# Optimization experiments

Measured on AMD Instinct MI355X. Metric: run time of the kernel, lower is better.

## Reference

```python
import jax, jax.numpy as jnp
import numpy as np

H = 512
B = 64
S = 2048
NUM_LAYERS = 1


def setup_inputs() -> dict:
    key = jax.random.key(0)
    ks = jax.random.split(key, 8)
    scale = 1.0 / np.sqrt(H)
    return {
        "hidden": jax.random.normal(ks[0], (NUM_LAYERS, B, H), dtype=jnp.float32),
        "encoder_outputs": jax.random.normal(ks[1], (B, S, H), dtype=jnp.float32),
        "U_w": jax.random.uniform(ks[2], (H, H), jnp.float32, -scale, scale),
        "U_b": jax.random.uniform(ks[3], (H,), jnp.float32, -scale, scale),
        "W_w": jax.random.uniform(ks[4], (H, H), jnp.float32, -scale, scale),
        "W_b": jax.random.uniform(ks[5], (H,), jnp.float32, -scale, scale),
        "V_w": jax.random.uniform(ks[6], (1, H), jnp.float32, -scale, scale),
        "V_b": jax.random.uniform(ks[7], (1,), jnp.float32, -scale, scale),
    }


def reference(hidden, encoder_outputs, U_w, U_b, W_w, W_b, V_w, V_b):
    # hidden: [L, B, H] -> take last layer, like hidden[-1]
    h = hidden[-1]  # [B, H]
    # Uatt(h): [B, H] -> broadcast over src_len
    u = h @ U_w.T + U_b            # [B, H]
    w = jnp.einsum('bsh,kh->bsk', encoder_outputs, W_w) + W_b  # [B, S, H]
    combined = jnp.tanh(u[:, None, :] + w)                     # [B, S, H]
    energy = jnp.einsum('bsh,h->bs', combined, V_w[0]) + V_b[0]  # [B, S]
    attn = jax.nn.softmax(energy, axis=1)                       # [B, S]
    context = jnp.einsum('bs,bsh->bh', attn, encoder_outputs)   # [B, H]
    return (context, attn)
```

## Files before the change

kernel.cpp:

```cpp
#include <hip/hip_runtime.h>
#include <hip/hip_bf16.h>

#define H 512
#define B 64
#define S 2048

typedef __bf16 bf16x8 __attribute__((ext_vector_type(8)));
typedef float f32x4 __attribute__((ext_vector_type(4)));
typedef unsigned int u32x4 __attribute__((ext_vector_type(4)));

__device__ __forceinline__ unsigned cvt2(float x, float y) {
    union { __hip_bfloat162 h; unsigned u; } cv;
    cv.h = __float22bfloat162_rn(make_float2(x, y));
    return cv.u;
}

__device__ __forceinline__ float fast_tanh(float x) {
    float e = __expf(2.0f * x);
    float r = __builtin_amdgcn_rcpf(e + 1.0f);
    return 1.0f - 2.0f * r;
}

__device__ __forceinline__ void gload_lds16(const void* g, void* l) {
    __builtin_amdgcn_global_load_lds(
        (const __attribute__((address_space(1))) unsigned int*)g,
        (__attribute__((address_space(3))) unsigned int*)l, 16, 0, 0);
}

__global__ __launch_bounds__(256) void w16_kernel(const float* __restrict__ Ww,
                                                  unsigned short* __restrict__ w16) {
    const int i = (blockIdx.x * 256 + threadIdx.x) * 8;
    float4 a = *(const float4*)(Ww + i);
    float4 b = *(const float4*)(Ww + i + 4);
    uint4 p;
    p.x = cvt2(a.x, a.y); p.y = cvt2(a.z, a.w);
    p.z = cvt2(b.x, b.y); p.w = cvt2(b.z, b.w);
    *(uint4*)(w16 + i) = p;
}

__global__ __launch_bounds__(256) void u_kernel(
        const float* __restrict__ hid, const float* __restrict__ Uw,
        const float* __restrict__ Ub, const float* __restrict__ Wb,
        float* __restrict__ u) {
    const int b = blockIdx.y;
    const int k = blockIdx.x * 4 + (threadIdx.x >> 6);
    const int lane = threadIdx.x & 63;
    const float4* wrow = (const float4*)(Uw + (size_t)k * H);
    const float4* hrow = (const float4*)(hid + (size_t)b * H);
    float4 w0 = wrow[lane * 2], w1 = wrow[lane * 2 + 1];
    float4 h0 = hrow[lane * 2], h1 = hrow[lane * 2 + 1];
    float acc = w0.x * h0.x + w0.y * h0.y + w0.z * h0.z + w0.w * h0.w
              + w1.x * h1.x + w1.y * h1.y + w1.z * h1.z + w1.w * h1.w;
    #pragma unroll
    for (int off = 1; off < 64; off <<= 1) acc += __shfl_xor(acc, off, 64);
    if (lane == 0) u[b * H + k] = acc + Ub[k] + Wb[k];
}

#define CN  32
#define NCH 16
#define CHB (CN * H * 2)

__global__ __launch_bounds__(256, 2) void energy_kernel(
        const float* __restrict__ enc, const unsigned short* __restrict__ w16,
        const float* __restrict__ Vw, const float* __restrict__ u,
        float* __restrict__ energy) {
    const int s0  = blockIdx.x * 128;
    const int b   = blockIdx.y;
    const int tid = threadIdx.x;
    const int wave = tid >> 6, lane = tid & 63;
    const int quad = lane >> 4, c = lane & 15;

    __shared__ unsigned char Bs[2][CHB];
    __shared__ float uS[H], vS[H];

    #pragma unroll
    for (int i = 0; i < 8; ++i) {
        const int row = i * 4 + wave;
        const int d   = (row << 10) + lane * 16;
        gload_lds16((const unsigned char*)w16 + (d ^ ((row & 7) << 4)),
                    &Bs[0][row << 10]);
    }

    for (int i = tid; i < H; i += 256) { uS[i] = u[b * H + i]; vS[i] = Vw[i]; }

    u32x4 apack[2][16];
    #pragma unroll
    for (int g = 0; g < 2; ++g) {
        const float* pa = enc + ((size_t)(b * S + s0 + wave * 32 + g * 16 + c)) * H + quad * 8;
        #pragma unroll
        for (int half = 0; half < 2; ++half) {
            float4 x0[8], x1[8];
            #pragma unroll
            for (int q = 0; q < 8; ++q) {
                const int t = half * 8 + q;
                x0[q] = *(const float4*)(pa + t * 32);
                x1[q] = *(const float4*)(pa + t * 32 + 4);
            }
            #pragma unroll
            for (int q = 0; q < 8; ++q) {
                u32x4 p;
                p[0] = cvt2(x0[q].x, x0[q].y); p[1] = cvt2(x0[q].z, x0[q].w);
                p[2] = cvt2(x1[q].x, x1[q].y); p[3] = cvt2(x1[q].z, x1[q].w);
                apack[g][half * 8 + q] = p;
            }
        }
    }
    #pragma unroll
    for (int g = 0; g < 2; ++g)
        #pragma unroll
        for (int t = 0; t < 16; ++t)
            asm volatile("" : "+v"(apack[g][t]));

    float esum[2][4] = {};
    const int mask = (c & 7) << 4;

    #pragma unroll 2
    for (int cc = 0; cc < NCH; ++cc) {
        const int buf = cc & 1;
        if (cc) __syncthreads();
        if (cc < NCH - 1) {
            const unsigned char* src = (const unsigned char*)w16 + (cc + 1) * CHB;
            #pragma unroll
            for (int i = 0; i < 8; ++i) {
                const int row = i * 4 + wave;
                const int d   = (row << 10) + lane * 16;
                gload_lds16(src + (d ^ ((row & 7) << 4)), &Bs[buf ^ 1][row << 10]);
            }
            asm volatile("s_waitcnt vmcnt(8)" ::: "memory");
        } else {
            asm volatile("s_waitcnt vmcnt(0)" ::: "memory");
        }
        __syncthreads();

        const unsigned char* bb = Bs[buf];
        f32x4 acc[2][2] = {};
        #pragma unroll
        for (int t = 0; t < 16; ++t) {
            const int base = t * 64 + quad * 16;
            bf16x8 b0 = *(const bf16x8*)(bb + ((( c       << 10) + base) ^ mask));
            bf16x8 b1 = *(const bf16x8*)(bb + ((((16 + c) << 10) + base) ^ mask));
            acc[0][0] = __builtin_amdgcn_mfma_f32_16x16x32_bf16(*(const bf16x8*)&apack[0][t], b0, acc[0][0], 0, 0, 0);
            acc[1][0] = __builtin_amdgcn_mfma_f32_16x16x32_bf16(*(const bf16x8*)&apack[1][t], b0, acc[1][0], 0, 0, 0);
            acc[0][1] = __builtin_amdgcn_mfma_f32_16x16x32_bf16(*(const bf16x8*)&apack[0][t], b1, acc[0][1], 0, 0, 0);
            acc[1][1] = __builtin_amdgcn_mfma_f32_16x16x32_bf16(*(const bf16x8*)&apack[1][t], b1, acc[1][1], 0, 0, 0);
        }
        #pragma unroll
        for (int ct = 0; ct < 2; ++ct) {
            const int col = cc * CN + ct * 16 + c;
            const float vv = vS[col], uu = uS[col];
            #pragma unroll
            for (int g = 0; g < 2; ++g)
                #pragma unroll
                for (int r = 0; r < 4; ++r)
                    esum[g][r] += vv * fast_tanh(uu + acc[g][ct][r]);
        }
    }

    #pragma unroll
    for (int g = 0; g < 2; ++g)
        #pragma unroll
        for (int r = 0; r < 4; ++r) {
            float e = esum[g][r];
            e += __shfl_xor(e, 1, 64);
            e += __shfl_xor(e, 2, 64);
            e += __shfl_xor(e, 4, 64);
            e += __shfl_xor(e, 8, 64);
            if (c == 0)
                energy[b * S + s0 + wave * 32 + g * 16 + quad * 4 + r] = e;
        }
}

__global__ void softmax_kernel(const float* __restrict__ energy, float* __restrict__ attn) {
    int b = blockIdx.x;
    int t = threadIdx.x;
    const float* e = energy + b * S;
    float v[8];
    float m = -1e30f;
    #pragma unroll
    for (int i = 0; i < 8; ++i) { v[i] = e[t + i * 256]; m = fmaxf(m, v[i]); }
    #pragma unroll
    for (int off = 1; off < 64; off <<= 1) m = fmaxf(m, __shfl_xor(m, off, 64));
    __shared__ float redm[4], reds[4];
    if ((t & 63) == 0) redm[t >> 6] = m;
    __syncthreads();
    m = fmaxf(fmaxf(redm[0], redm[1]), fmaxf(redm[2], redm[3]));
    float s = 0.f;
    #pragma unroll
    for (int i = 0; i < 8; ++i) { v[i] = __expf(v[i] - m); s += v[i]; }
    #pragma unroll
    for (int off = 1; off < 64; off <<= 1) s += __shfl_xor(s, off, 64);
    if ((t & 63) == 0) reds[t >> 6] = s;
    __syncthreads();
    float inv = 1.0f / (reds[0] + reds[1] + reds[2] + reds[3]);
    #pragma unroll
    for (int i = 0; i < 8; ++i) attn[b * S + t + i * 256] = v[i] * inv;
}

#define CCH 128
__global__ __launch_bounds__(256) void context_kernel(
        const float* __restrict__ enc, const float* __restrict__ attn,
        float* __restrict__ ctx) {
    const int b  = blockIdx.x >> 4;
    const int ch = blockIdx.x & 15;
    const int t  = threadIdx.x;
    const int grp = t >> 7;
    const int ln  = t & 127;
    __shared__ float aS[CCH];
    __shared__ float red[H];
    if (t < CCH) aS[t] = attn[b * S + ch * CCH + t];
    __syncthreads();
    const float* ebase = enc + ((size_t)(b * S + ch * CCH) + grp * 64) * H + ln * 4;
    float4 acc = make_float4(0.f, 0.f, 0.f, 0.f);
    #pragma unroll 8
    for (int s = 0; s < 64; ++s) {
        const float a = aS[grp * 64 + s];
        const float4 e = *(const float4*)(ebase + (size_t)s * H);
        acc.x += a * e.x; acc.y += a * e.y; acc.z += a * e.z; acc.w += a * e.w;
    }
    if (grp == 0) *(float4*)&red[ln * 4] = acc;
    __syncthreads();
    if (grp == 1) {
        const float4 r = *(const float4*)&red[ln * 4];
        atomicAdd(&ctx[b * H + ln * 4 + 0], acc.x + r.x);
        atomicAdd(&ctx[b * H + ln * 4 + 1], acc.y + r.y);
        atomicAdd(&ctx[b * H + ln * 4 + 2], acc.z + r.z);
        atomicAdd(&ctx[b * H + ln * 4 + 3], acc.w + r.w);
    }
}

extern "C" void kernel_launch(void* const* d_in, const int* in_sizes, int n_in,
                              void* d_out, int out_size, void* d_ws, size_t ws_size,
                              hipStream_t stream) {
    (void)in_sizes; (void)n_in; (void)out_size; (void)ws_size;
    const float* hid = (const float*)d_in[0];
    const float* enc = (const float*)d_in[1];
    const float* Uw  = (const float*)d_in[2];
    const float* Ub  = (const float*)d_in[3];
    const float* Ww  = (const float*)d_in[4];
    const float* Wb  = (const float*)d_in[5];
    const float* Vw  = (const float*)d_in[6];

    float* out_ctx  = (float*)d_out;
    float* out_attn = out_ctx + B * H;
    float* energy   = (float*)d_ws;
    float* u        = energy + B * S;
    unsigned short* w16 = (unsigned short*)(u + B * H);

    hipMemsetAsync(d_out, 0, (size_t)B * H * sizeof(float), stream);

    w16_kernel<<<dim3(H * H / (256 * 8)), 256, 0, stream>>>(Ww, w16);
    u_kernel<<<dim3(H / 4, B), 256, 0, stream>>>(hid, Uw, Ub, Wb, u);
    energy_kernel<<<dim3(S / 128, B), 256, 0, stream>>>(enc, w16, Vw, u, energy);
    softmax_kernel<<<B, 256, 0, stream>>>(energy, out_attn);
    context_kernel<<<B * 16, 256, 0, stream>>>(enc, out_attn, out_ctx);
}
```

Baseline: 479.8 us.

## Split energy block across 8 waves with 16 rows each to raise occupancy

The energy kernel now runs 512 threads per block. Each wave owns 16 sequence rows instead of 32, which halves the A-fragment registers and accumulators per wave, and the launch bound asks for 4 blocks per CU. The W chunk loads are spread over 8 waves (4 loads each) with a matching vmcnt, and s_setprio is raised around the MFMA loop. The aim is more resident waves to hide LDS and global latency. In exchange, each B fragment read from LDS now feeds only 2 MFMAs instead of 4, so LDS read traffic per FLOP doubles.

Result: slower. 490.6 us (+2.3%).

```diff
diff --git a/kernel.cpp b/kernel.cpp
--- a/kernel.cpp
+++ b/kernel.cpp
@@ -60,7 +60,7 @@
 #define NCH 16
 #define CHB (CN * H * 2)
 
-__global__ __launch_bounds__(256, 2) void energy_kernel(
+__global__ __launch_bounds__(512, 4) void energy_kernel(
         const float* __restrict__ enc, const unsigned short* __restrict__ w16,
         const float* __restrict__ Vw, const float* __restrict__ u,
         float* __restrict__ energy) {
@@ -74,19 +74,19 @@
     __shared__ float uS[H], vS[H];
 
     #pragma unroll
-    for (int i = 0; i < 8; ++i) {
-        const int row = i * 4 + wave;
+    for (int i = 0; i < 4; ++i) {
+        const int row = i * 8 + wave;
         const int d   = (row << 10) + lane * 16;
         gload_lds16((const unsigned char*)w16 + (d ^ ((row & 7) << 4)),
                     &Bs[0][row << 10]);
     }
 
-    for (int i = tid; i < H; i += 256) { uS[i] = u[b * H + i]; vS[i] = Vw[i]; }
-
-    u32x4 apack[2][16];
-    #pragma unroll
-    for (int g = 0; g < 2; ++g) {
-        const float* pa = enc + ((size_t)(b * S + s0 + wave * 32 + g * 16 + c)) * H + quad * 8;
+    uS[tid] = u[b * H + tid];
+    vS[tid] = Vw[tid];
+
+    u32x4 apack[16];
+    {
+        const float* pa = enc + ((size_t)(b * S + s0 + wave * 16 + c)) * H + quad * 8;
         #pragma unroll
         for (int half = 0; half < 2; ++half) {
             float4 x0[8], x1[8];
@@ -101,17 +101,13 @@
                 u32x4 p;
                 p[0] = cvt2(x0[q].x, x0[q].y); p[1] = cvt2(x0[q].z, x0[q].w);
                 p[2] = cvt2(x1[q].x, x1[q].y); p[3] = cvt2(x1[q].z, x1[q].w);
-                apack[g][half * 8 + q] = p;
+                apack[half * 8 + q] = p;
+                asm volatile("" : "+v"(apack[half * 8 + q]));
             }
         }
     }
-    #pragma unroll
-    for (int g = 0; g < 2; ++g)
-        #pragma unroll
-        for (int t = 0; t < 16; ++t)
-            asm volatile("" : "+v"(apack[g][t]));
-
-    float esum[2][4] = {};
+
+    float esum[4] = {};
     const int mask = (c & 7) << 4;
 
     #pragma unroll 2
@@ -121,53 +117,49 @@
         if (cc < NCH - 1) {
             const unsigned char* src = (const unsigned char*)w16 + (cc + 1) * CHB;
             #pragma unroll
-            for (int i = 0; i < 8; ++i) {
-                const int row = i * 4 + wave;
+            for (int i = 0; i < 4; ++i) {
+                const int row = i * 8 + wave;
                 const int d   = (row << 10) + lane * 16;
                 gload_lds16(src + (d ^ ((row & 7) << 4)), &Bs[buf ^ 1][row << 10]);
             }
-            asm volatile("s_waitcnt vmcnt(8)" ::: "memory");
+            asm volatile("s_waitcnt vmcnt(4)" ::: "memory");
         } else {
             asm volatile("s_waitcnt vmcnt(0)" ::: "memory");
         }
         __syncthreads();
 
         const unsigned char* bb = Bs[buf];
-        f32x4 acc[2][2] = {};
+        f32x4 acc[2] = {};
+        __builtin_amdgcn_s_setprio(1);
         #pragma unroll
         for (int t = 0; t < 16; ++t) {
             const int base = t * 64 + quad * 16;
             bf16x8 b0 = *(const bf16x8*)(bb + ((( c       << 10) + base) ^ mask));
             bf16x8 b1 = *(const bf16x8*)(bb + ((((16 + c) << 10) + base) ^ mask));
-            acc[0][0] = __builtin_amdgcn_mfma_f32_16x16x32_bf16(*(const bf16x8*)&apack[0][t], b0, acc[0][0], 0, 0, 0);
-            acc[1][0] = __builtin_amdgcn_mfma_f32_16x16x32_bf16(*(const bf16x8*)&apack[1][t], b0, acc[1][0], 0, 0, 0);
-            acc[0][1] = __builtin_amdgcn_mfma_f32_16x16x32_bf16(*(const bf16x8*)&apack[0][t], b1, acc[0][1], 0, 0, 0);
-            acc[1][1] = __builtin_amdgcn_mfma_f32_16x16x32_bf16(*(const bf16x8*)&apack[1][t], b1, acc[1][1], 0, 0, 0);
-        }
+            acc[0] = __builtin_amdgcn_mfma_f32_16x16x32_bf16(*(const bf16x8*)&apack[t], b0, acc[0], 0, 0, 0);
+            acc[1] = __builtin_amdgcn_mfma_f32_16x16x32_bf16(*(const bf16x8*)&apack[t], b1, acc[1], 0, 0, 0);
+        }
+        __builtin_amdgcn_s_setprio(0);
         #pragma unroll
         for (int ct = 0; ct < 2; ++ct) {
             const int col = cc * CN + ct * 16 + c;
             const float vv = vS[col], uu = uS[col];
             #pragma unroll
-            for (int g = 0; g < 2; ++g)
-                #pragma unroll
-                for (int r = 0; r < 4; ++r)
-                    esum[g][r] += vv * fast_tanh(uu + acc[g][ct][r]);
-        }
-    }
-
-    #pragma unroll
-    for (int g = 0; g < 2; ++g)
-        #pragma unroll
-        for (int r = 0; r < 4; ++r) {
-            float e = esum[g][r];
-            e += __shfl_xor(e, 1, 64);
-            e += __shfl_xor(e, 2, 64);
-            e += __shfl_xor(e, 4, 64);
-            e += __shfl_xor(e, 8, 64);
-            if (c == 0)
-                energy[b * S + s0 + wave * 32 + g * 16 + quad * 4 + r] = e;
-        }
+            for (int r = 0; r < 4; ++r)
+                esum[r] += vv * fast_tanh(uu + acc[ct][r]);
+        }
+    }
+
+    #pragma unroll
+    for (int r = 0; r < 4; ++r) {
+        float e = esum[r];
+        e += __shfl_xor(e, 1, 64);
+        e += __shfl_xor(e, 2, 64);
+        e += __shfl_xor(e, 4, 64);
+        e += __shfl_xor(e, 8, 64);
+        if (c == 0)
+            energy[b * S + s0 + wave * 16 + quad * 4 + r] = e;
+    }
 }
 
 __global__ void softmax_kernel(const float* __restrict__ energy, float* __restrict__ attn) {
@@ -250,7 +242,7 @@
 
     w16_kernel<<<dim3(H * H / (256 * 8)), 256, 0, stream>>>(Ww, w16);
     u_kernel<<<dim3(H / 4, B), 256, 0, stream>>>(hid, Uw, Ub, Wb, u);
-    energy_kernel<<<dim3(S / 128, B), 256, 0, stream>>>(enc, w16, Vw, u, energy);
+    energy_kernel<<<dim3(S / 128, B), 512, 0, stream>>>(enc, w16, Vw, u, energy);
     softmax_kernel<<<B, 256, 0, stream>>>(energy, out_attn);
     context_kernel<<<B * 16, 256, 0, stream>>>(enc, out_attn, out_ctx);
 }
```

## Retile energy GEMM as 2x2 wave grid with streamed A through LDS

Applied to the files above, without the earlier changes.

The energy kernel's GEMM is retiled. Previously each wave kept its 32 encoder rows fully in registers as bf16 and streamed the W weights through large 32KB LDS chunks. Now the 128x512 A tile is streamed in 32-wide K slices through LDS, with a 2x2 wave layout where each wave computes 64x64 outputs, and B is staged in small 8KB double buffers. Per-wave partial energies are combined through a shared reduction buffer. The aim is to cut register and LDS pressure so occupancy can go to 3 blocks, and to raise MFMA reuse per fragment load. The cost is two barriers per K step and reloading the A slices for each of the 4 N tiles.

After: 560.5 us. +16.8%, slower.

```diff
diff --git a/kernel.cpp b/kernel.cpp
--- a/kernel.cpp
+++ b/kernel.cpp
@@ -7,7 +7,6 @@
 
 typedef __bf16 bf16x8 __attribute__((ext_vector_type(8)));
 typedef float f32x4 __attribute__((ext_vector_type(4)));
-typedef unsigned int u32x4 __attribute__((ext_vector_type(4)));
 
 __device__ __forceinline__ unsigned cvt2(float x, float y) {
     union { __hip_bfloat162 h; unsigned u; } cv;
@@ -56,11 +55,7 @@
     if (lane == 0) u[b * H + k] = acc + Ub[k] + Wb[k];
 }
 
-#define CN  32
-#define NCH 16
-#define CHB (CN * H * 2)
-
-__global__ __launch_bounds__(256, 2) void energy_kernel(
+__global__ __launch_bounds__(256, 3) void energy_kernel(
         const float* __restrict__ enc, const unsigned short* __restrict__ w16,
         const float* __restrict__ Vw, const float* __restrict__ u,
         float* __restrict__ energy) {
@@ -69,105 +64,130 @@
     const int tid = threadIdx.x;
     const int wave = tid >> 6, lane = tid & 63;
     const int quad = lane >> 4, c = lane & 15;
-
-    __shared__ unsigned char Bs[2][CHB];
+    const int wr = wave >> 1, wc = wave & 1;
+
+    __shared__ unsigned short As[128][40];
+    __shared__ unsigned char  Bsh[2][8192];
     __shared__ float uS[H], vS[H];
-
-    #pragma unroll
-    for (int i = 0; i < 8; ++i) {
-        const int row = i * 4 + wave;
-        const int d   = (row << 10) + lane * 16;
-        gload_lds16((const unsigned char*)w16 + (d ^ ((row & 7) << 4)),
-                    &Bs[0][row << 10]);
-    }
-
+    __shared__ float red[128];
+
+    const int brow_l = lane >> 2;
+    const int bcs    = lane & 3;
+
+    const unsigned char* wb = (const unsigned char*)w16;
+
+    #define STAGE_B(nt, kt, buf)                                               \
+        _Pragma("unroll")                                                      \
+        for (int i_ = 0; i_ < 2; ++i_) {                                       \
+            const int row_ = wave * 32 + i_ * 16 + brow_l;                     \
+            gload_lds16(wb + ((size_t)((nt) * 128 + row_) * H + (kt) * 32) * 2 \
+                           + ((bcs ^ (row_ & 3)) * 16),                        \
+                        &Bsh[buf][(wave * 32 + i_ * 16) * 64]);                \
+        }
+
+    const int r  = tid >> 1;
+    const int hh = (tid & 1) * 16;
+    const float* pa = enc + ((size_t)(b * S + s0 + r)) * H + hh;
+
+    float4 ar0, ar1, ar2, ar3;
+    #define LOAD_A(kt) {                                                       \
+        const float* p_ = pa + (kt) * 32;                                      \
+        ar0 = *(const float4*)(p_);                                            \
+        ar1 = *(const float4*)(p_ + 4);                                        \
+        ar2 = *(const float4*)(p_ + 8);                                        \
+        ar3 = *(const float4*)(p_ + 12);                                       \
+    }
+
+    STAGE_B(0, 0, 0);
+    LOAD_A(0);
     for (int i = tid; i < H; i += 256) { uS[i] = u[b * H + i]; vS[i] = Vw[i]; }
 
-    u32x4 apack[2][16];
-    #pragma unroll
-    for (int g = 0; g < 2; ++g) {
-        const float* pa = enc + ((size_t)(b * S + s0 + wave * 32 + g * 16 + c)) * H + quad * 8;
-        #pragma unroll
-        for (int half = 0; half < 2; ++half) {
-            float4 x0[8], x1[8];
-            #pragma unroll
-            for (int q = 0; q < 8; ++q) {
-                const int t = half * 8 + q;
-                x0[q] = *(const float4*)(pa + t * 32);
-                x1[q] = *(const float4*)(pa + t * 32 + 4);
-            }
-            #pragma unroll
-            for (int q = 0; q < 8; ++q) {
-                u32x4 p;
-                p[0] = cvt2(x0[q].x, x0[q].y); p[1] = cvt2(x0[q].z, x0[q].w);
-                p[2] = cvt2(x1[q].x, x1[q].y); p[3] = cvt2(x1[q].z, x1[q].w);
-                apack[g][half * 8 + q] = p;
-            }
-        }
-    }
-    #pragma unroll
-    for (int g = 0; g < 2; ++g)
-        #pragma unroll
-        for (int t = 0; t < 16; ++t)
-            asm volatile("" : "+v"(apack[g][t]));
-
-    float esum[2][4] = {};
-    const int mask = (c & 7) << 4;
-
-    #pragma unroll 2
-    for (int cc = 0; cc < NCH; ++cc) {
-        const int buf = cc & 1;
-        if (cc) __syncthreads();
-        if (cc < NCH - 1) {
-            const unsigned char* src = (const unsigned char*)w16 + (cc + 1) * CHB;
-            #pragma unroll
-            for (int i = 0; i < 8; ++i) {
-                const int row = i * 4 + wave;
-                const int d   = (row << 10) + lane * 16;
-                gload_lds16(src + (d ^ ((row & 7) << 4)), &Bs[buf ^ 1][row << 10]);
-            }
-            asm volatile("s_waitcnt vmcnt(8)" ::: "memory");
-        } else {
-            asm volatile("s_waitcnt vmcnt(0)" ::: "memory");
-        }
-        __syncthreads();
-
-        const unsigned char* bb = Bs[buf];
-        f32x4 acc[2][2] = {};
-        #pragma unroll
-        for (int t = 0; t < 16; ++t) {
-            const int base = t * 64 + quad * 16;
-            bf16x8 b0 = *(const bf16x8*)(bb + ((( c       << 10) + base) ^ mask));
-            bf16x8 b1 = *(const bf16x8*)(bb + ((((16 + c) << 10) + base) ^ mask));
-            acc[0][0] = __builtin_amdgcn_mfma_f32_16x16x32_bf16(*(const bf16x8*)&apack[0][t], b0, acc[0][0], 0, 0, 0);
-            acc[1][0] = __builtin_amdgcn_mfma_f32_16x16x32_bf16(*(const bf16x8*)&apack[1][t], b0, acc[1][0], 0, 0, 0);
-            acc[0][1] = __builtin_amdgcn_mfma_f32_16x16x32_bf16(*(const bf16x8*)&apack[0][t], b1, acc[0][1], 0, 0, 0);
-            acc[1][1] = __builtin_amdgcn_mfma_f32_16x16x32_bf16(*(const bf16x8*)&apack[1][t], b1, acc[1][1], 0, 0, 0);
-        }
-        #pragma unroll
-        for (int ct = 0; ct < 2; ++ct) {
-            const int col = cc * CN + ct * 16 + c;
+    float esum[4][4] = {};
+    const f32x4 fzero = {0.f, 0.f, 0.f, 0.f};
+
+    for (int nt = 0; nt < 4; ++nt) {
+        f32x4 acc[4][4];
+        #pragma unroll
+        for (int i = 0; i < 4; ++i)
+            #pragma unroll
+            for (int j = 0; j < 4; ++j) acc[i][j] = fzero;
+
+        for (int kt = 0; kt < 16; ++kt) {
+            const int buf = kt & 1;
+            __syncthreads();
+            {
+                uint4 p0, p1;
+                p0.x = cvt2(ar0.x, ar0.y); p0.y = cvt2(ar0.z, ar0.w);
+                p0.z = cvt2(ar1.x, ar1.y); p0.w = cvt2(ar1.z, ar1.w);
+                p1.x = cvt2(ar2.x, ar2.y); p1.y = cvt2(ar2.z, ar2.w);
+                p1.z = cvt2(ar3.x, ar3.y); p1.w = cvt2(ar3.z, ar3.w);
+                *(uint4*)&As[r][hh]     = p0;
+                *(uint4*)&As[r][hh + 8] = p1;
+            }
+            __syncthreads();
+            const int tn = nt * 16 + kt + 1;
+            if (tn < 64) {
+                STAGE_B(tn >> 4, tn & 15, buf ^ 1);
+                LOAD_A(tn & 15);
+            }
+            bf16x8 af[4], bf[4];
+            #pragma unroll
+            for (int i = 0; i < 4; ++i)
+                af[i] = *(const bf16x8*)&As[wr * 64 + i * 16 + c][quad * 8];
+            #pragma unroll
+            for (int j = 0; j < 4; ++j) {
+                const int R = wc * 64 + j * 16 + c;
+                bf[j] = *(const bf16x8*)&Bsh[buf][R * 64 + ((quad ^ (c & 3)) * 16)];
+            }
+            #pragma unroll
+            for (int i = 0; i < 4; ++i)
+                #pragma unroll
+                for (int j = 0; j < 4; ++j)
+                    acc[i][j] = __builtin_amdgcn_mfma_f32_16x16x32_bf16(af[i], bf[j], acc[i][j], 0, 0, 0);
+        }
+        #pragma unroll
+        for (int j = 0; j < 4; ++j) {
+            const int col = nt * 128 + wc * 64 + j * 16 + c;
             const float vv = vS[col], uu = uS[col];
             #pragma unroll
-            for (int g = 0; g < 2; ++g)
+            for (int i = 0; i < 4; ++i)
                 #pragma unroll
-                for (int r = 0; r < 4; ++r)
-                    esum[g][r] += vv * fast_tanh(uu + acc[g][ct][r]);
-        }
-    }
-
-    #pragma unroll
-    for (int g = 0; g < 2; ++g)
-        #pragma unroll
-        for (int r = 0; r < 4; ++r) {
-            float e = esum[g][r];
+                for (int rr = 0; rr < 4; ++rr)
+                    esum[i][rr] += vv * fast_tanh(uu + acc[i][j][rr]);
+        }
+    }
+
+    #pragma unroll
+    for (int i = 0; i < 4; ++i)
+        #pragma unroll
+        for (int rr = 0; rr < 4; ++rr) {
+            float e = esum[i][rr];
             e += __shfl_xor(e, 1, 64);
             e += __shfl_xor(e, 2, 64);
             e += __shfl_xor(e, 4, 64);
             e += __shfl_xor(e, 8, 64);
-            if (c == 0)
-                energy[b * S + s0 + wave * 32 + g * 16 + quad * 4 + r] = e;
-        }
+            esum[i][rr] = e;
+        }
+    __syncthreads();
+    if (wc == 0 && c == 0) {
+        #pragma unroll
+        for (int i = 0; i < 4; ++i)
+            #pragma unroll
+            for (int rr = 0; rr < 4; ++rr)
+                red[wr * 64 + i * 16 + quad * 4 + rr] = esum[i][rr];
+    }
+    __syncthreads();
+    if (wc == 1 && c == 0) {
+        #pragma unroll
+        for (int i = 0; i < 4; ++i)
+            #pragma unroll
+            for (int rr = 0; rr < 4; ++rr) {
+                const int row = wr * 64 + i * 16 + quad * 4 + rr;
+                energy[b * S + s0 + row] = red[row] + esum[i][rr];
+            }
+    }
+    #undef STAGE_B
+    #undef LOAD_A
 }
 
 __global__ void softmax_kernel(const float* __restrict__ energy, float* __restrict__ attn) {
```
